# Kernel tuning notes

Hardware: AMD Instinct MI355X
Metric: run time of the kernel (lower is better)

The kernel has to match this reference:

```python
import jax, jax.numpy as jnp
import numpy as np

N, Lq, Lk, D = 4, 2048, 2048, 1024
H, DH = 16, 64  # n_heads, projection_dim
NEG_INF = jnp.float32(-1e30)


def setup_inputs() -> dict:
    key = jax.random.key(0)
    ks = jax.random.split(key, 6)
    query = jax.random.normal(ks[0], (N, Lq, D), dtype=jnp.float32)
    key_t = jax.random.normal(ks[1], (N, Lk, D), dtype=jnp.float32)
    s = 1.0 / np.sqrt(D)
    Wq = jax.random.normal(ks[2], (D, D), dtype=jnp.float32) * s
    Wk = jax.random.normal(ks[3], (D, D), dtype=jnp.float32) * s
    Wv = jax.random.normal(ks[4], (D, D), dtype=jnp.float32) * s
    # causal mask: True where attention is forbidden (j > i)
    mask = jnp.triu(jnp.ones((Lq, Lk), dtype=bool), k=1)
    # per-sample valid lengths in [1024, 2048); padding at the tail
    valid_len = jax.random.randint(ks[5], (N,), Lk // 2, Lk)
    padding_mask = jnp.arange(Lk)[None, :] >= valid_len[:, None]  # (N, Lk) bool
    return {"query": query, "key": key_t, "Wq": Wq, "Wk": Wk, "Wv": Wv,
            "mask": mask, "padding_mask": padding_mask}


def reference(query, key, Wq, Wk, Wv, mask, padding_mask):
    n, lq, _ = query.shape
    lk = key.shape[1]
    # torch Linear (no bias): x @ W.T ; split heads -> (N, H, L, DH)
    q = (query @ Wq.T).reshape(n, lq, H, DH).transpose(0, 2, 1, 3)
    k = (key @ Wk.T).reshape(n, lk, H, DH).transpose(0, 2, 1, 3)
    v = (key @ Wv.T).reshape(n, lk, H, DH).transpose(0, 2, 1, 3)
    # per-sample scaling: sqrt(number of non-padded keys) (module quirk, not sqrt(d))
    valid = jnp.sum(~padding_mask, axis=-1).astype(query.dtype)  # (N,)
    scaling = jnp.sqrt(valid)[:, None, None, None]
    score = jnp.einsum('nhqd,nhkd->nhqk', q, k) / scaling
    score = jnp.where(mask[None, None, :, :], NEG_INF, score)
    score = jnp.where(padding_mask[:, None, None, :], NEG_INF, score)
    attn = jax.nn.softmax(score, axis=-1)
    out = jnp.einsum('nhqk,nhkd->nhqd', attn, v)
    return out.transpose(0, 2, 1, 3).reshape(n, lq, H * DH)
```

## Files before the change

### kernel.cpp

```cpp
#include <hip/hip_runtime.h>
#include <hip/hip_bf16.h>
#include <math.h>


#define N_S 4
#define LQ 2048
#define LK 2048
#define DM 1024
#define NHEAD 16
#define DHEAD 64

typedef __attribute__((ext_vector_type(8))) short short8;
typedef __attribute__((ext_vector_type(4))) float f32x4;

typedef const __attribute__((address_space(1))) void* gptr_t;
typedef __attribute__((address_space(3))) void* lptr_t;

#define GLOAD_LDS(g, l) \
    __builtin_amdgcn_global_load_lds((gptr_t)(const void*)(g), (lptr_t)(void*)(l), 16, 0, 0)

static __device__ __forceinline__ unsigned int pkbf(float a, float b) {
    __hip_bfloat162 h = __float22bfloat162_rn(make_float2(a, b));
    unsigned int u;
    __builtin_memcpy(&u, &h, 4);
    return u;
}

static __device__ __forceinline__ f32x4 zero4() {
    f32x4 v; v[0] = 0.f; v[1] = 0.f; v[2] = 0.f; v[3] = 0.f; return v;
}

__global__ void meta_kernel(const void* __restrict__ pm,
                            int* __restrict__ valid_out,
                            float* __restrict__ scale_out) {
    __shared__ int okInt, hasPair, okF32;
    __shared__ int counts[4];
    int t = threadIdx.x;
    if (t == 0) { okInt = 1; hasPair = 0; okF32 = 1; }
    if (t < 4) counts[t] = 0;
    __syncthreads();

    const unsigned int* w = (const unsigned int*)pm;
    int bad_int = 0, pair = 0, bad_f32 = 0;
    for (int i = t; i < 2048; i += 256) {
        unsigned int v = w[i];
        if (v > 1u) bad_int = 1;
        if (v == 0x3F803F80u) pair = 1;
        if (v != 0u && v != 0x3F800000u) bad_f32 = 1;
    }
    if (bad_int) okInt = 0;
    if (pair)    hasPair = 1;
    if (bad_f32) okF32 = 0;
    __syncthreads();

    int mode = okInt ? 0 : (hasPair ? 1 : (okF32 ? 2 : 3));
    for (int n = 0; n < 4; n++) {
        int cnt = 0;
        for (int j = t; j < LK; j += 256) {
            int idx = n * LK + j;
            bool z;
            if (mode == 0)      z = (((const int*)pm)[idx] == 0);
            else if (mode == 1) z = (((const unsigned short*)pm)[idx] == 0);
            else if (mode == 2) z = (w[idx] == 0u);
            else                z = (((const unsigned char*)pm)[idx] == 0);
            cnt += z ? 1 : 0;
        }
        atomicAdd(&counts[n], cnt);
    }
    __syncthreads();
    if (t < 4) {
        int c = counts[t] > 0 ? counts[t] : 1;
        valid_out[t] = c;
        scale_out[t] = 1.0f / sqrtf((float)c);
    }
}

static __device__ __forceinline__ void conv16(const float* src,
                                              unsigned short* dst, size_t idx) {
    f32x4 a0 = *(const f32x4*)(src + idx);
    f32x4 a1 = *(const f32x4*)(src + idx + 4);
    f32x4 a2 = *(const f32x4*)(src + idx + 8);
    f32x4 a3 = *(const f32x4*)(src + idx + 12);
    uint4 u0, u1;
    u0.x = pkbf(a0[0], a0[1]); u0.y = pkbf(a0[2], a0[3]);
    u0.z = pkbf(a1[0], a1[1]); u0.w = pkbf(a1[2], a1[3]);
    u1.x = pkbf(a2[0], a2[1]); u1.y = pkbf(a2[2], a2[3]);
    u1.z = pkbf(a3[0], a3[1]); u1.w = pkbf(a3[2], a3[3]);
    *(uint4*)(void*)(dst + idx) = u0;
    *(uint4*)(void*)(dst + idx + 8) = u1;
}

__global__ __launch_bounds__(256) void convw_kernel(
    const float* __restrict__ Wq, const float* __restrict__ Wk,
    const float* __restrict__ Wv,
    unsigned short* __restrict__ Wqb, unsigned short* __restrict__ Wkb,
    unsigned short* __restrict__ Wvb)
{
    int z = blockIdx.y;
    const float* src = (z == 0) ? Wq : ((z == 1) ? Wk : Wv);
    unsigned short* dst = (z == 0) ? Wqb : ((z == 1) ? Wkb : Wvb);
    conv16(src, dst, ((size_t)blockIdx.x * 256 + threadIdx.x) * 16);
}

__global__ __launch_bounds__(256) void convx_kernel(
    const float* __restrict__ src, unsigned short* __restrict__ dst)
{
    conv16(src, dst, ((size_t)blockIdx.x * 256 + threadIdx.x) * 16);
}

__global__ __launch_bounds__(256) void proj_bf16_kernel(
    const unsigned short* __restrict__ Xb,
    const unsigned short* __restrict__ Wqb, const unsigned short* __restrict__ Wkb,
    const unsigned short* __restrict__ Wvb,
    const float* __restrict__ scal,
    unsigned short* __restrict__ Qb, unsigned short* __restrict__ Kb,
    unsigned short* __restrict__ Vt, int zbase)
{
    int z = blockIdx.z + zbase;
    const unsigned short* W = (z == 0) ? Wqb : ((z == 1) ? Wkb : Wvb);

    __shared__ unsigned short Xls[128 * 32];
    __shared__ unsigned short Wls[128 * 32];

    int t = threadIdx.x;
    int wave = t >> 6, lane = t & 63;
    int l15 = lane & 15, quad = lane >> 4;
    int wa = wave >> 1, wb = wave & 1;
    int m0 = blockIdx.x << 7, n0 = blockIdx.y << 7;

    int srow = t >> 2;
    int sg = ((t & 3) ^ (srow & 3)) << 3;
    const unsigned short* gX0 = Xb + (size_t)(m0 + srow) * DM + sg;
    const unsigned short* gX1 = Xb + (size_t)(m0 + 64 + srow) * DM + sg;
    const unsigned short* gW0 = W + (size_t)(n0 + srow) * DM + sg;
    const unsigned short* gW1 = W + (size_t)(n0 + 64 + srow) * DM + sg;

    f32x4 acc[4][4];
    #pragma unroll
    for (int i = 0; i < 4; i++)
        #pragma unroll
        for (int j = 0; j < 4; j++) acc[i][j] = zero4();

    int aoff = ((quad ^ (l15 & 3)) << 3);
    const unsigned short* Abuf = (z < 2) ? Wls : Xls;
    const unsigned short* Bbuf = (z < 2) ? Xls : Wls;

    for (int kk = 0; kk < DM; kk += 32) {
        __syncthreads();
        GLOAD_LDS(gX0 + kk, Xls + wave * 512);
        GLOAD_LDS(gX1 + kk, Xls + 2048 + wave * 512);
        GLOAD_LDS(gW0 + kk, Wls + wave * 512);
        GLOAD_LDS(gW1 + kk, Wls + 2048 + wave * 512);
        __syncthreads();

        short8 af[4], bf[4];
        #pragma unroll
        for (int ai = 0; ai < 4; ai++)
            af[ai] = *(const short8*)(const void*)(
                Abuf + ((wa * 64 + ai * 16 + l15) << 5) + aoff);
        #pragma unroll
        for (int bi = 0; bi < 4; bi++)
            bf[bi] = *(const short8*)(const void*)(
                Bbuf + ((wb * 64 + bi * 16 + l15) << 5) + aoff);
        #pragma unroll
        for (int ai = 0; ai < 4; ai++)
            #pragma unroll
            for (int bi = 0; bi < 4; bi++)
                acc[ai][bi] = __builtin_amdgcn_mfma_f32_16x16x32_bf16(
                    af[ai], bf[bi], acc[ai][bi], 0, 0, 0);
    }

    if (z < 2) {
        unsigned short* O = (z == 0) ? Qb : Kb;
        #pragma unroll
        for (int bi = 0; bi < 4; bi++) {
            int token = m0 + wb * 64 + bi * 16 + l15;
            float qs = 1.0f;
            if (z == 0) qs = scal[token >> 11] * 1.44269504f;
            #pragma unroll
            for (int ai = 0; ai < 4; ai++) {
                int feat = n0 + wa * 64 + ai * 16 + quad * 4;
                float v0 = acc[ai][bi][0], v1 = acc[ai][bi][1];
                float v2 = acc[ai][bi][2], v3 = acc[ai][bi][3];
                if (z == 0) { v0 *= qs; v1 *= qs; v2 *= qs; v3 *= qs; }
                uint2 u;
                u.x = pkbf(v0, v1);
                u.y = pkbf(v2, v3);
                *(uint2*)(void*)(O + (size_t)token * DM + feat) = u;
            }
        }
    } else {
        #pragma unroll
        for (int ai = 0; ai < 4; ai++) {
            int token0 = m0 + wa * 64 + ai * 16 + quad * 4;
            int n = token0 >> 11, tl = token0 & 2047;
            #pragma unroll
            for (int bi = 0; bi < 4; bi++) {
                int feat = n0 + wb * 64 + bi * 16 + l15;
                uint2 u;
                u.x = pkbf(acc[ai][bi][0], acc[ai][bi][1]);
                u.y = pkbf(acc[ai][bi][2], acc[ai][bi][3]);
                *(uint2*)(void*)(Vt + ((size_t)n * DM + feat) * LK + tl) = u;
            }
        }
    }
}

__global__ __launch_bounds__(256) void proj_f32_kernel(
    const float* __restrict__ Xq, const float* __restrict__ Xk,
    const unsigned short* __restrict__ Wqb, const unsigned short* __restrict__ Wkb,
    const unsigned short* __restrict__ Wvb,
    const float* __restrict__ scal,
    unsigned short* __restrict__ Qb, unsigned short* __restrict__ Kb,
    unsigned short* __restrict__ Vt)
{
    int z = blockIdx.z;
    const float* X = (z == 0) ? Xq : Xk;
    const unsigned short* W = (z == 0) ? Wqb : ((z == 1) ? Wkb : Wvb);

    __shared__ unsigned short Xls[128 * 32];
    __shared__ unsigned short Wls[128 * 32];

    int t = threadIdx.x;
    int wave = t >> 6, lane = t & 63;
    int l15 = lane & 15, quad = lane >> 4;
    int wa = wave >> 1, wb = wave & 1;
    int m0 = blockIdx.x << 7, n0 = blockIdx.y << 7;

    int arow = t >> 1, ah = t & 1;
    int ag0 = ((2 * ah)     ^ (arow & 3)) << 3;
    int ag1 = ((2 * ah + 1) ^ (arow & 3)) << 3;
    const float* gX = X + (size_t)(m0 + arow) * DM;
    unsigned short* lX = Xls + arow * 32 + ah * 16;

    int brow = t >> 2;
    int bg = ((t & 3) ^ (brow & 3)) << 3;
    const unsigned short* gW0 = W + (size_t)(n0 + brow) * DM + bg;
    const unsigned short* gW1 = W + (size_t)(n0 + 64 + brow) * DM + bg;

    f32x4 acc[4][4];
    #pragma unroll
    for (int i = 0; i < 4; i++)
        #pragma unroll
        for (int j = 0; j < 4; j++) acc[i][j] = zero4();

    int aoff = ((quad ^ (l15 & 3)) << 3);

    f32x4 an0 = *(const f32x4*)(gX + ag0);
    f32x4 an1 = *(const f32x4*)(gX + ag0 + 4);
    f32x4 an2 = *(const f32x4*)(gX + ag1);
    f32x4 an3 = *(const f32x4*)(gX + ag1 + 4);

    const unsigned short* Abuf = (z < 2) ? Wls : Xls;
    const unsigned short* Bbuf = (z < 2) ? Xls : Wls;

    for (int kk = 0; kk < DM; kk += 32) {
        __syncthreads();
        GLOAD_LDS(gW0 + kk, Wls + wave * 512);
        GLOAD_LDS(gW1 + kk, Wls + 2048 + wave * 512);
        uint4 ua, ub;
        ua.x = pkbf(an0[0], an0[1]); ua.y = pkbf(an0[2], an0[3]);
        ua.z = pkbf(an1[0], an1[1]); ua.w = pkbf(an1[2], an1[3]);
        ub.x = pkbf(an2[0], an2[1]); ub.y = pkbf(an2[2], an2[3]);
        ub.z = pkbf(an3[0], an3[1]); ub.w = pkbf(an3[2], an3[3]);
        *(uint4*)(void*)(lX)     = ua;
        *(uint4*)(void*)(lX + 8) = ub;
        __syncthreads();

        if (kk + 32 < DM) {
            an0 = *(const f32x4*)(gX + kk + 32 + ag0);
            an1 = *(const f32x4*)(gX + kk + 32 + ag0 + 4);
            an2 = *(const f32x4*)(gX + kk + 32 + ag1);
            an3 = *(const f32x4*)(gX + kk + 32 + ag1 + 4);
        }

        short8 af[4], bf[4];
        #pragma unroll
        for (int ai = 0; ai < 4; ai++)
            af[ai] = *(const short8*)(const void*)(
                Abuf + ((wa * 64 + ai * 16 + l15) << 5) + aoff);
        #pragma unroll
        for (int bi = 0; bi < 4; bi++)
            bf[bi] = *(const short8*)(const void*)(
                Bbuf + ((wb * 64 + bi * 16 + l15) << 5) + aoff);
        #pragma unroll
        for (int ai = 0; ai < 4; ai++)
            #pragma unroll
            for (int bi = 0; bi < 4; bi++)
                acc[ai][bi] = __builtin_amdgcn_mfma_f32_16x16x32_bf16(
                    af[ai], bf[bi], acc[ai][bi], 0, 0, 0);
    }

    if (z < 2) {
        unsigned short* O = (z == 0) ? Qb : Kb;
        #pragma unroll
        for (int bi = 0; bi < 4; bi++) {
            int token = m0 + wb * 64 + bi * 16 + l15;
            float qs = 1.0f;
            if (z == 0) qs = scal[token >> 11] * 1.44269504f;
            #pragma unroll
            for (int ai = 0; ai < 4; ai++) {
                int feat = n0 + wa * 64 + ai * 16 + quad * 4;
                float v0 = acc[ai][bi][0], v1 = acc[ai][bi][1];
                float v2 = acc[ai][bi][2], v3 = acc[ai][bi][3];
                if (z == 0) { v0 *= qs; v1 *= qs; v2 *= qs; v3 *= qs; }
                uint2 u;
                u.x = pkbf(v0, v1);
                u.y = pkbf(v2, v3);
                *(uint2*)(void*)(O + (size_t)token * DM + feat) = u;
            }
        }
    } else {
        #pragma unroll
        for (int ai = 0; ai < 4; ai++) {
            int token0 = m0 + wa * 64 + ai * 16 + quad * 4;
            int n = token0 >> 11, tl = token0 & 2047;
            #pragma unroll
            for (int bi = 0; bi < 4; bi++) {
                int feat = n0 + wb * 64 + bi * 16 + l15;
                uint2 u;
                u.x = pkbf(acc[ai][bi][0], acc[ai][bi][1]);
                u.y = pkbf(acc[ai][bi][2], acc[ai][bi][3]);
                *(uint2*)(void*)(Vt + ((size_t)n * DM + feat) * LK + tl) = u;
            }
        }
    }
}

__global__ __launch_bounds__(256) void attn_kernel(
    const unsigned short* __restrict__ Qb, const unsigned short* __restrict__ Kb,
    const unsigned short* __restrict__ Vt,
    const int* __restrict__ valid_arr,
    float* __restrict__ out)
{
    __shared__ unsigned short Kls[2][64 * 64];
    __shared__ unsigned short Pls[4][2][16 * 72];

    int bx = blockIdx.x;
    int nh = blockIdx.y;
    int n = nh >> 4, h = nh & 15;
    int tA = bx, tB = 31 - bx;

    int valid = valid_arr[n];
    int tvalid = (valid + 63) >> 6;
    int TlA = (tA + 1 < tvalid) ? tA + 1 : tvalid;
    int TlB = (tB + 1 < tvalid) ? tB + 1 : tvalid;

    int t = threadIdx.x;
    int wave = t >> 6, lane = t & 63;
    int l15 = lane & 15, quad = lane >> 4;

    int qyA = tA * 64 + wave * 16 + l15;
    int qyB = tB * 64 + wave * 16 + l15;
    int qw0A = tA * 64 + wave * 16;
    int qw0B = tB * 64 + wave * 16;

    const unsigned short* QrowA = Qb + ((size_t)n * LQ + qyA) * DM + h * DHEAD;
    const unsigned short* QrowB = Qb + ((size_t)n * LQ + qyB) * DM + h * DHEAD;
    short8 qfA0 = *(const short8*)(const void*)(QrowA + quad * 8);
    short8 qfA1 = *(const short8*)(const void*)(QrowA + 32 + quad * 8);
    short8 qfB0 = *(const short8*)(const void*)(QrowB + quad * 8);
    short8 qfB1 = *(const short8*)(const void*)(QrowB + 32 + quad * 8);

    f32x4 OA[4], OB[4];
    #pragma unroll
    for (int i = 0; i < 4; i++) { OA[i] = zero4(); OB[i] = zero4(); }
    f32x4 LAcc = zero4(), LBcc = zero4();

    short8 onesf;
    #pragma unroll
    for (int i = 0; i < 8; i++) onesf[i] = (short)0x3F80;

    const unsigned short* Kbase = Kb + (size_t)n * LK * DM + h * DHEAD;
    const unsigned short* Vbase = Vt + ((size_t)n * DM + h * DHEAD) * LK;
    unsigned short* plsA = &Pls[wave][0][0];
    unsigned short* plsB = &Pls[wave][1][0];

    int srow0 = t >> 3;
    int sgk   = (((t & 7) ^ (srow0 & 7)) << 3);

    GLOAD_LDS(Kbase + (size_t)srow0 * DM + sgk,        &Kls[0][0] + wave * 512);
    GLOAD_LDS(Kbase + (size_t)(32 + srow0) * DM + sgk, &Kls[0][0] + 2048 + wave * 512);

    for (int kt = 0; kt < TlB; kt++) {
        int jb = kt << 6;
        int cur = kt & 1;
        bool doA = (kt < TlA);

        __syncthreads();

        f32x4 sA[4], sB[4];
        #pragma unroll
        for (int cb = 0; cb < 4; cb++) {
            const unsigned short* krow = &Kls[cur][0] + ((cb * 16 + l15) << 6);
            short8 kf0 = *(const short8*)(const void*)(krow + ((quad ^ (l15 & 7)) << 3));
            short8 kf1 = *(const short8*)(const void*)(krow + (((4 + quad) ^ (l15 & 7)) << 3));
            f32x4 sb = zero4();
            sb = __builtin_amdgcn_mfma_f32_16x16x32_bf16(kf0, qfB0, sb, 0, 0, 0);
            sb = __builtin_amdgcn_mfma_f32_16x16x32_bf16(kf1, qfB1, sb, 0, 0, 0);
            sB[cb] = sb;
            if (doA) {
                f32x4 sa = zero4();
                sa = __builtin_amdgcn_mfma_f32_16x16x32_bf16(kf0, qfA0, sa, 0, 0, 0);
                sa = __builtin_amdgcn_mfma_f32_16x16x32_bf16(kf1, qfA1, sa, 0, 0, 0);
                sA[cb] = sa;
            }
        }

        short8 vf0[4], vf1[4];
        #pragma unroll
        for (int cb = 0; cb < 4; cb++) {
            vf0[cb] = *(const short8*)(const void*)(
                Vbase + (size_t)(cb * 16 + l15) * LK + jb + quad * 8);
            vf1[cb] = *(const short8*)(const void*)(
                Vbase + (size_t)(cb * 16 + l15) * LK + jb + 32 + quad * 8);
        }
        if (kt + 1 < TlB) {
            int jb2 = jb + 64;
            GLOAD_LDS(Kbase + (size_t)(jb2 + srow0) * DM + sgk,
                      &Kls[1 - cur][0] + wave * 512);
            GLOAD_LDS(Kbase + (size_t)(jb2 + 32 + srow0) * DM + sgk,
                      &Kls[1 - cur][0] + 2048 + wave * 512);
        }

        if (jb + 63 > qw0B || jb + 64 > valid) {
            #pragma unroll
            for (int cb = 0; cb < 4; cb++) {
                int jb2 = jb + cb * 16 + quad * 4;
                #pragma unroll
                for (int r = 0; r < 4; r++) {
                    int j = jb2 + r;
                    if (j > qyB || j >= valid) sB[cb][r] = -1e30f;
                }
            }
        }
        #pragma unroll
        for (int cb = 0; cb < 4; cb++) {
            uint2 u;
            u.x = pkbf(__builtin_amdgcn_exp2f(sB[cb][0]),
                       __builtin_amdgcn_exp2f(sB[cb][1]));
            u.y = pkbf(__builtin_amdgcn_exp2f(sB[cb][2]),
                       __builtin_amdgcn_exp2f(sB[cb][3]));
            *(uint2*)(void*)(plsB + l15 * 72 + cb * 16 + quad * 4) = u;
        }
        if (doA) {
            if (jb + 63 > qw0A || jb + 64 > valid) {
                #pragma unroll
                for (int cb = 0; cb < 4; cb++) {
                    int jb2 = jb + cb * 16 + quad * 4;
                    #pragma unroll
                    for (int r = 0; r < 4; r++) {
                        int j = jb2 + r;
                        if (j > qyA || j >= valid) sA[cb][r] = -1e30f;
                    }
                }
            }
            #pragma unroll
            for (int cb = 0; cb < 4; cb++) {
                uint2 u;
                u.x = pkbf(__builtin_amdgcn_exp2f(sA[cb][0]),
                           __builtin_amdgcn_exp2f(sA[cb][1]));
                u.y = pkbf(__builtin_amdgcn_exp2f(sA[cb][2]),
                           __builtin_amdgcn_exp2f(sA[cb][3]));
                *(uint2*)(void*)(plsA + l15 * 72 + cb * 16 + quad * 4) = u;
            }
        }

        short8 pfB0 = *(const short8*)(const void*)(plsB + l15 * 72 + quad * 8);
        short8 pfB1 = *(const short8*)(const void*)(plsB + l15 * 72 + 32 + quad * 8);
        #pragma unroll
        for (int cb = 0; cb < 4; cb++) {
            OB[cb] = __builtin_amdgcn_mfma_f32_16x16x32_bf16(pfB0, vf0[cb], OB[cb], 0, 0, 0);
            OB[cb] = __builtin_amdgcn_mfma_f32_16x16x32_bf16(pfB1, vf1[cb], OB[cb], 0, 0, 0);
        }
        LBcc = __builtin_amdgcn_mfma_f32_16x16x32_bf16(pfB0, onesf, LBcc, 0, 0, 0);
        LBcc = __builtin_amdgcn_mfma_f32_16x16x32_bf16(pfB1, onesf, LBcc, 0, 0, 0);
        if (doA) {
            short8 pfA0 = *(const short8*)(const void*)(plsA + l15 * 72 + quad * 8);
            short8 pfA1 = *(const short8*)(const void*)(plsA + l15 * 72 + 32 + quad * 8);
            #pragma unroll
            for (int cb = 0; cb < 4; cb++) {
                OA[cb] = __builtin_amdgcn_mfma_f32_16x16x32_bf16(pfA0, vf0[cb], OA[cb], 0, 0, 0);
                OA[cb] = __builtin_amdgcn_mfma_f32_16x16x32_bf16(pfA1, vf1[cb], OA[cb], 0, 0, 0);
            }
            LAcc = __builtin_amdgcn_mfma_f32_16x16x32_bf16(pfA0, onesf, LAcc, 0, 0, 0);
            LAcc = __builtin_amdgcn_mfma_f32_16x16x32_bf16(pfA1, onesf, LAcc, 0, 0, 0);
        }
    }

    float* obase = out + ((size_t)n * LQ) * DM + h * DHEAD;
    #pragma unroll
    for (int r = 0; r < 4; r++) {
        float iA = 1.0f / LAcc[r];
        float iB = 1.0f / LBcc[r];
        int rowA = tA * 64 + wave * 16 + quad * 4 + r;
        int rowB = tB * 64 + wave * 16 + quad * 4 + r;
        #pragma unroll
        for (int cb = 0; cb < 4; cb++) {
            obase[(size_t)rowA * DM + cb * 16 + l15] = OA[cb][r] * iA;
            obase[(size_t)rowB * DM + cb * 16 + l15] = OB[cb][r] * iB;
        }
    }
}

extern "C" void kernel_launch(void* const* d_in, const int* in_sizes, int n_in,
                              void* d_out, int out_size, void* d_ws, size_t ws_size,
                              hipStream_t stream)
{
    (void)in_sizes; (void)n_in; (void)out_size;

    const float* query = (const float*)d_in[0];
    const float* key   = (const float*)d_in[1];
    const float* Wq    = (const float*)d_in[2];
    const float* Wk    = (const float*)d_in[3];
    const float* Wv    = (const float*)d_in[4];
    const void* pmask  = d_in[6];

    char* ws = (char*)d_ws;
    unsigned short* Qb  = (unsigned short*)(ws);
    unsigned short* Kb  = (unsigned short*)(ws + (size_t)16 * 1024 * 1024);
    unsigned short* Vt  = (unsigned short*)(ws + (size_t)32 * 1024 * 1024);
    int*   valid = (int*)  (ws + (size_t)48 * 1024 * 1024);
    float* scal  = (float*)(ws + (size_t)48 * 1024 * 1024 + 64);
    unsigned short* Wqb = (unsigned short*)(ws + (size_t)48 * 1024 * 1024 + 4096);
    unsigned short* Wkb = Wqb + (size_t)DM * DM;
    unsigned short* Wvb = Wkb + (size_t)DM * DM;
    unsigned short* Xb  = Wvb + (size_t)DM * DM;
    size_t need = (size_t)(48 * 1024 * 1024) + 4096
                + 3 * (size_t)DM * DM * 2 + (size_t)N_S * LQ * DM * 2;

    meta_kernel<<<1, 256, 0, stream>>>(pmask, valid, scal);
    convw_kernel<<<dim3(256, 3), 256, 0, stream>>>(Wq, Wk, Wv, Wqb, Wkb, Wvb);

    if (ws_size >= need) {
        convx_kernel<<<2048, 256, 0, stream>>>(query, Xb);
        proj_bf16_kernel<<<dim3(64, 8, 1), 256, 0, stream>>>(
            Xb, Wqb, Wkb, Wvb, scal, Qb, Kb, Vt, 0);
        convx_kernel<<<2048, 256, 0, stream>>>(key, Xb);
        proj_bf16_kernel<<<dim3(64, 8, 2), 256, 0, stream>>>(
            Xb, Wqb, Wkb, Wvb, scal, Qb, Kb, Vt, 1);
    } else {
        proj_f32_kernel<<<dim3(64, 8, 3), 256, 0, stream>>>(
            query, key, Wqb, Wkb, Wvb, scal, Qb, Kb, Vt);
    }

    attn_kernel<<<dim3(16, 64), 256, 0, stream>>>(Qb, Kb, Vt, valid,
                                                  (float*)d_out);
}
```

Before: 352.7 us.

## Build P fragments in registers via permlane swaps and fuse Q/K/V projection launches

In the attention loop, the exp'd probabilities are no longer staged through LDS and read back in MFMA A-operand layout. Instead, v_permlane32/16_swap instructions rearrange the packed bf16 values across lanes directly in registers, which removes LDS stores and loads plus their latency. The Pls shared array is dropped and launch bounds request 4 blocks per CU for higher occupancy. When the workspace is large enough, query and key are converted to bf16 in one launch and a single projection launch covers Q, K and V, cutting kernel launches and improving grid fill, at the cost of a second bf16 input buffer.

```diff
diff --git a/kernel.cpp b/kernel.cpp
--- a/kernel.cpp
+++ b/kernel.cpp
@@ -108,8 +108,17 @@
     conv16(src, dst, ((size_t)blockIdx.x * 256 + threadIdx.x) * 16);
 }
 
+__global__ __launch_bounds__(256) void convx2_kernel(
+    const float* __restrict__ q, const float* __restrict__ k,
+    unsigned short* __restrict__ dq, unsigned short* __restrict__ dk)
+{
+    const float* src = blockIdx.y ? k : q;
+    unsigned short* dst = blockIdx.y ? dk : dq;
+    conv16(src, dst, ((size_t)blockIdx.x * 256 + threadIdx.x) * 16);
+}
+
 __global__ __launch_bounds__(256) void proj_bf16_kernel(
-    const unsigned short* __restrict__ Xb,
+    const unsigned short* __restrict__ XbQ, const unsigned short* __restrict__ XbK,
     const unsigned short* __restrict__ Wqb, const unsigned short* __restrict__ Wkb,
     const unsigned short* __restrict__ Wvb,
     const float* __restrict__ scal,
@@ -118,6 +127,7 @@
 {
     int z = blockIdx.z + zbase;
     const unsigned short* W = (z == 0) ? Wqb : ((z == 1) ? Wkb : Wvb);
+    const unsigned short* Xb = (z == 0) ? XbQ : XbK;
 
     __shared__ unsigned short Xls[128 * 32];
     __shared__ unsigned short Wls[128 * 32];
@@ -327,14 +337,13 @@
     }
 }
 
-__global__ __launch_bounds__(256) void attn_kernel(
+__global__ __launch_bounds__(256, 4) void attn_kernel(
     const unsigned short* __restrict__ Qb, const unsigned short* __restrict__ Kb,
     const unsigned short* __restrict__ Vt,
     const int* __restrict__ valid_arr,
     float* __restrict__ out)
 {
     __shared__ unsigned short Kls[2][64 * 64];
-    __shared__ unsigned short Pls[4][2][16 * 72];
 
     int bx = blockIdx.x;
     int nh = blockIdx.y;
@@ -373,8 +382,6 @@
 
     const unsigned short* Kbase = Kb + (size_t)n * LK * DM + h * DHEAD;
     const unsigned short* Vbase = Vt + ((size_t)n * DM + h * DHEAD) * LK;
-    unsigned short* plsA = &Pls[wave][0][0];
-    unsigned short* plsB = &Pls[wave][1][0];
 
     int srow0 = t >> 3;
     int sgk   = (((t & 7) ^ (srow0 & 7)) << 3);
@@ -434,15 +441,39 @@
                 }
             }
         }
+        short8 pfB0, pfB1;
+        {
+            unsigned int lo[4], hi[4];
+            #pragma unroll
+            for (int cb = 0; cb < 4; cb++) {
+                lo[cb] = pkbf(__builtin_amdgcn_exp2f(sB[cb][0]),
+                              __builtin_amdgcn_exp2f(sB[cb][1]));
+                hi[cb] = pkbf(__builtin_amdgcn_exp2f(sB[cb][2]),
+                              __builtin_amdgcn_exp2f(sB[cb][3]));
+            }
+            asm("v_permlane32_swap_b32 %0, %1" : "+v"(lo[0]), "+v"(lo[1]));
+            asm("v_permlane32_swap_b32 %0, %1" : "+v"(hi[0]), "+v"(hi[1]));
+            asm("v_permlane32_swap_b32 %0, %1" : "+v"(lo[2]), "+v"(lo[3]));
+            asm("v_permlane32_swap_b32 %0, %1" : "+v"(hi[2]), "+v"(hi[3]));
+            asm("v_permlane16_swap_b32 %0, %1" : "+v"(lo[0]), "+v"(lo[1]));
+            asm("v_permlane16_swap_b32 %0, %1" : "+v"(hi[0]), "+v"(hi[1]));
+            asm("v_permlane16_swap_b32 %0, %1" : "+v"(lo[2]), "+v"(lo[3]));
+            asm("v_permlane16_swap_b32 %0, %1" : "+v"(hi[2]), "+v"(hi[3]));
+            uint4 w0, w1;
+            w0.x = lo[0]; w0.y = hi[0]; w0.z = lo[1]; w0.w = hi[1];
+            w1.x = lo[2]; w1.y = hi[2]; w1.z = lo[3]; w1.w = hi[3];
+            __builtin_memcpy(&pfB0, &w0, 16);
+            __builtin_memcpy(&pfB1, &w1, 16);
+        }
+
         #pragma unroll
         for (int cb = 0; cb < 4; cb++) {
-            uint2 u;
-            u.x = pkbf(__builtin_amdgcn_exp2f(sB[cb][0]),
-                       __builtin_amdgcn_exp2f(sB[cb][1]));
-            u.y = pkbf(__builtin_amdgcn_exp2f(sB[cb][2]),
-                       __builtin_amdgcn_exp2f(sB[cb][3]));
-            *(uint2*)(void*)(plsB + l15 * 72 + cb * 16 + quad * 4) = u;
-        }
+            OB[cb] = __builtin_amdgcn_mfma_f32_16x16x32_bf16(pfB0, vf0[cb], OB[cb], 0, 0, 0);
+            OB[cb] = __builtin_amdgcn_mfma_f32_16x16x32_bf16(pfB1, vf1[cb], OB[cb], 0, 0, 0);
+        }
+        LBcc = __builtin_amdgcn_mfma_f32_16x16x32_bf16(pfB0, onesf, LBcc, 0, 0, 0);
+        LBcc = __builtin_amdgcn_mfma_f32_16x16x32_bf16(pfB1, onesf, LBcc, 0, 0, 0);
+
         if (doA) {
             if (jb + 63 > qw0A || jb + 64 > valid) {
                 #pragma unroll
@@ -455,29 +486,30 @@
                     }
                 }
             }
-            #pragma unroll
-            for (int cb = 0; cb < 4; cb++) {
-                uint2 u;
-                u.x = pkbf(__builtin_amdgcn_exp2f(sA[cb][0]),
-                           __builtin_amdgcn_exp2f(sA[cb][1]));
-                u.y = pkbf(__builtin_amdgcn_exp2f(sA[cb][2]),
-                           __builtin_amdgcn_exp2f(sA[cb][3]));
-                *(uint2*)(void*)(plsA + l15 * 72 + cb * 16 + quad * 4) = u;
-            }
-        }
-
-        short8 pfB0 = *(const short8*)(const void*)(plsB + l15 * 72 + quad * 8);
-        short8 pfB1 = *(const short8*)(const void*)(plsB + l15 * 72 + 32 + quad * 8);
-        #pragma unroll
-        for (int cb = 0; cb < 4; cb++) {
-            OB[cb] = __builtin_amdgcn_mfma_f32_16x16x32_bf16(pfB0, vf0[cb], OB[cb], 0, 0, 0);
-            OB[cb] = __builtin_amdgcn_mfma_f32_16x16x32_bf16(pfB1, vf1[cb], OB[cb], 0, 0, 0);
-        }
-        LBcc = __builtin_amdgcn_mfma_f32_16x16x32_bf16(pfB0, onesf, LBcc, 0, 0, 0);
-        LBcc = __builtin_amdgcn_mfma_f32_16x16x32_bf16(pfB1, onesf, LBcc, 0, 0, 0);
-        if (doA) {
-            short8 pfA0 = *(const short8*)(const void*)(plsA + l15 * 72 + quad * 8);
-            short8 pfA1 = *(const short8*)(const void*)(plsA + l15 * 72 + 32 + quad * 8);
+            short8 pfA0, pfA1;
+            {
+                unsigned int lo[4], hi[4];
+                #pragma unroll
+                for (int cb = 0; cb < 4; cb++) {
+                    lo[cb] = pkbf(__builtin_amdgcn_exp2f(sA[cb][0]),
+                                  __builtin_amdgcn_exp2f(sA[cb][1]));
+                    hi[cb] = pkbf(__builtin_amdgcn_exp2f(sA[cb][2]),
+                                  __builtin_amdgcn_exp2f(sA[cb][3]));
+                }
+                asm("v_permlane32_swap_b32 %0, %1" : "+v"(lo[0]), "+v"(lo[1]));
+                asm("v_permlane32_swap_b32 %0, %1" : "+v"(hi[0]), "+v"(hi[1]));
+                asm("v_permlane32_swap_b32 %0, %1" : "+v"(lo[2]), "+v"(lo[3]));
+                asm("v_permlane32_swap_b32 %0, %1" : "+v"(hi[2]), "+v"(hi[3]));
+                asm("v_permlane16_swap_b32 %0, %1" : "+v"(lo[0]), "+v"(lo[1]));
+                asm("v_permlane16_swap_b32 %0, %1" : "+v"(hi[0]), "+v"(hi[1]));
+                asm("v_permlane16_swap_b32 %0, %1" : "+v"(lo[2]), "+v"(lo[3]));
+                asm("v_permlane16_swap_b32 %0, %1" : "+v"(hi[2]), "+v"(hi[3]));
+                uint4 w0, w1;
+                w0.x = lo[0]; w0.y = hi[0]; w0.z = lo[1]; w0.w = hi[1];
+                w1.x = lo[2]; w1.y = hi[2]; w1.z = lo[3]; w1.w = hi[3];
+                __builtin_memcpy(&pfA0, &w0, 16);
+                __builtin_memcpy(&pfA1, &w1, 16);
+            }
             #pragma unroll
             for (int cb = 0; cb < 4; cb++) {
                 OA[cb] = __builtin_amdgcn_mfma_f32_16x16x32_bf16(pfA0, vf0[cb], OA[cb], 0, 0, 0);
@@ -525,20 +557,28 @@
     unsigned short* Wqb = (unsigned short*)(ws + (size_t)48 * 1024 * 1024 + 4096);
     unsigned short* Wkb = Wqb + (size_t)DM * DM;
     unsigned short* Wvb = Wkb + (size_t)DM * DM;
-    unsigned short* Xb  = Wvb + (size_t)DM * DM;
-    size_t need = (size_t)(48 * 1024 * 1024) + 4096
-                + 3 * (size_t)DM * DM * 2 + (size_t)N_S * LQ * DM * 2;
+    unsigned short* XbQ = Wvb + (size_t)DM * DM;
+    unsigned short* XbK = XbQ + (size_t)N_S * LQ * DM;
+
+    size_t xbytes      = (size_t)N_S * LQ * DM * 2;
+    size_t need_phased = (size_t)(48 * 1024 * 1024) + 4096
+                       + 3 * (size_t)DM * DM * 2 + xbytes;
+    size_t need_full   = need_phased + xbytes;
 
     meta_kernel<<<1, 256, 0, stream>>>(pmask, valid, scal);
     convw_kernel<<<dim3(256, 3), 256, 0, stream>>>(Wq, Wk, Wv, Wqb, Wkb, Wvb);
 
-    if (ws_size >= need) {
-        convx_kernel<<<2048, 256, 0, stream>>>(query, Xb);
+    if (ws_size >= need_full) {
+        convx2_kernel<<<dim3(2048, 2), 256, 0, stream>>>(query, key, XbQ, XbK);
+        proj_bf16_kernel<<<dim3(64, 8, 3), 256, 0, stream>>>(
+            XbQ, XbK, Wqb, Wkb, Wvb, scal, Qb, Kb, Vt, 0);
+    } else if (ws_size >= need_phased) {
+        convx_kernel<<<2048, 256, 0, stream>>>(query, XbQ);
         proj_bf16_kernel<<<dim3(64, 8, 1), 256, 0, stream>>>(
-            Xb, Wqb, Wkb, Wvb, scal, Qb, Kb, Vt, 0);
-        convx_kernel<<<2048, 256, 0, stream>>>(key, Xb);
+            XbQ, XbQ, Wqb, Wkb, Wvb, scal, Qb, Kb, Vt, 0);
+        convx_kernel<<<2048, 256, 0, stream>>>(key, XbQ);
         proj_bf16_kernel<<<dim3(64, 8, 2), 256, 0, stream>>>(
-            Xb, Wqb, Wkb, Wvb, scal, Qb, Kb, Vt, 1);
+            XbQ, XbQ, Wqb, Wkb, Wvb, scal, Qb, Kb, Vt, 1);
     } else {
         proj_f32_kernel<<<dim3(64, 8, 3), 256, 0, stream>>>(
             query, key, Wqb, Wkb, Wvb, scal, Qb, Kb, Vt);
```

New measurement: 367.8 us. 4.3% more time.
